# Performance work log

Measured on AMD Instinct MI355X. Metric: run time of the kernel, lower is better.

## Reference

```python
import jax, jax.numpy as jnp
import numpy as np

# Dimensions
B = 8        # batch
T = 2048     # subtokens per sample
G = 1024     # pooled tokens (nodes + edges) per sample
NN = 600     # node slots per sample (seg_ids > 0)
NE = 424     # edge slots per sample (seg_ids < 0); NN + NE == G
D = 1024     # d_model == pretrained_dim (BART-large), so need_proj is False
V = 53587    # AMRBART vocab size
L = 2        # graph_layer_configs.nlayers


def setup_inputs() -> dict:
    key = jax.random.key(0)
    ks = jax.random.split(key, 8)
    scale = 0.02
    tokens_ids = jax.random.randint(ks[0], (B, T), 0, V, dtype=jnp.int32)
    # ragged token_splits encoded as segment ids; uniform groups of size T//G == 2
    token_group_ids = jnp.broadcast_to(
        jnp.arange(T, dtype=jnp.int32) // (T // G), (B, T))
    # seg_ids: +1 for node slots, -1 for edge slots (nodes-first layout, no pad)
    seg_ids = jnp.broadcast_to(
        jnp.concatenate([jnp.ones(NN, jnp.int32), -jnp.ones(NE, jnp.int32)]),
        (B, G))
    # torch-geometric style global edge index over batch-concatenated nodes
    src = jax.random.randint(ks[1], (B, NE), 0, NN, dtype=jnp.int32)
    dst = jax.random.randint(ks[2], (B, NE), 0, NN, dtype=jnp.int32)
    offs = (jnp.arange(B, dtype=jnp.int32) * NN)[:, None]
    edge_index = jnp.stack([(src + offs).reshape(-1), (dst + offs).reshape(-1)], 0)
    embedding_table = jax.random.normal(ks[3], (V, D), dtype=jnp.float32) * scale
    W_msg = jax.random.normal(ks[4], (L, D, D), dtype=jnp.float32) * scale
    W_upd = jax.random.normal(ks[5], (L, D, D), dtype=jnp.float32) * scale
    W_edge = jax.random.normal(ks[6], (L, D, D), dtype=jnp.float32) * scale
    return {"tokens_ids": tokens_ids, "token_group_ids": token_group_ids,
            "seg_ids": seg_ids, "edge_index": edge_index,
            "embedding_table": embedding_table,
            "W_msg": W_msg, "W_upd": W_upd, "W_edge": W_edge}


def reference(tokens_ids, token_group_ids, seg_ids, edge_index,
              embedding_table, W_msg, W_upd, W_edge):
    # 1) embedding lookup: [B, T, D]
    token_feats = embedding_table[tokens_ids]
    # 2) ragged subtoken mean-pool (torch.split + mean) via segment_sum
    seg_sum = jax.vmap(lambda x, ids: jax.ops.segment_sum(x, ids, num_segments=G))
    sums = seg_sum(token_feats, token_group_ids)                       # [B, G, D]
    counts = seg_sum(jnp.ones((B, T, 1), token_feats.dtype), token_group_ids)
    pooled = sums / jnp.maximum(counts, 1.0)                           # [B, G, D]
    # 3) gather node/edge feats (seg_ids layout is nodes-first, statically known)
    nodes = pooled[:, :NN].reshape(B * NN, D)
    edges = pooled[:, NN:].reshape(B * NE, D)
    src, dst = edge_index[0], edge_index[1]
    # 4) graph layers: edge-conditioned message passing with residuals
    for l in range(L):
        msg = jax.nn.relu((nodes[src] + edges) @ W_msg[l])             # [B*NE, D]
        agg = jax.ops.segment_sum(msg, dst, num_segments=B * NN)       # [B*NN, D]
        new_edges = edges + (nodes[src] + nodes[dst]) @ W_edge[l]
        nodes = nodes + agg @ W_upd[l]
        edges = new_edges
    # 5) scatter back into padded [B, G, D] tensor (boolean-mask scatter in torch)
    all_feats = jnp.concatenate(
        [nodes.reshape(B, NN, D), edges.reshape(B, NE, D)], axis=1)
    return all_feats
```

## Files before the change

### kernel.cpp

```cpp
#include <hip/hip_runtime.h>

constexpr int kB  = 8;
constexpr int kT  = 2048;
constexpr int kG  = 1024;
constexpr int kNN = 600;
constexpr int kNE = 424;
constexpr int kD  = 1024;
constexpr int kL  = 2;
constexpr int kBNN = kB * kNN;
constexpr int kBNE = kB * kNE;
static_assert(kBNE % 64 == 0, "M tiles exact");

typedef __attribute__((ext_vector_type(4))) float f32x4;
typedef __attribute__((ext_vector_type(8))) short bf16x8;
typedef __attribute__((address_space(1))) const void gas_t;
typedef __attribute__((address_space(3))) void las_t;

__device__ __forceinline__ unsigned short f2bf(float x) {
    union { float f; unsigned u; } v; v.f = x;
    unsigned r = v.u + 0x7FFF + ((v.u >> 16) & 1);
    return (unsigned short)(r >> 16);
}

__device__ __forceinline__ void glds16(const void* g, void* l) {
    __builtin_amdgcn_global_load_lds((gas_t*)g, (las_t*)l, 16, 0, 0);
}

__device__ __forceinline__ size_t edge_out_off(int row) {
    int b = row / kNE, r = row - b * kNE;
    return ((size_t)(b * kG + kNN + r)) * kD;
}
__device__ __forceinline__ size_t node_out_off(int n) {
    int b = n / kNN, g = n - b * kNN;
    return ((size_t)(b * kG + g)) * kD;
}

__global__ __launch_bounds__(256) void prep_kernel(const int* __restrict__ tokens,
                                                   const int* __restrict__ gids,
                                                   const float* __restrict__ emb,
                                                   float* __restrict__ nodes,
                                                   float* __restrict__ edges,
                                                   const float* __restrict__ Wm,
                                                   const float* __restrict__ Wu,
                                                   const float* __restrict__ We,
                                                   unsigned short* __restrict__ Wt) {
    __shared__ float tbuf[32][33];
    int bx = blockIdx.x;
    if (bx < kB * kG) {
        int b = bx >> 10, g = bx & (kG - 1);
        int d = threadIdx.x * 4;
        const int* row = gids + (size_t)b * kT;
        int lo = 0, hi = kT;
        while (lo < hi) { int m = (lo + hi) >> 1; if (row[m] < g) lo = m + 1; else hi = m; }
        int s = lo; hi = kT;
        while (lo < hi) { int m = (lo + hi) >> 1; if (row[m] <= g) lo = m + 1; else hi = m; }
        int e = lo;
        float4 acc = make_float4(0.f, 0.f, 0.f, 0.f);
        for (int t = s; t < e; ++t) {
            int tok = tokens[(size_t)b * kT + t];
            const float4 v = *(const float4*)(emb + (size_t)tok * kD + d);
            acc.x += v.x; acc.y += v.y; acc.z += v.z; acc.w += v.w;
        }
        int c = e - s;
        float sc = 1.0f / (float)(c > 0 ? c : 1);
        acc.x *= sc; acc.y *= sc; acc.z *= sc; acc.w *= sc;
        float* dstp = (g < kNN)
            ? (nodes + (size_t)(b * kNN + g) * kD + d)
            : (edges + (size_t)(b * kNE + (g - kNN)) * kD + d);
        *(float4*)dstp = acc;
    } else {
        int idx = bx - kB * kG;
        int z = idx >> 10;
        int rem = idx & 1023;
        int n0 = (rem & 31) * 32, k0 = (rem >> 5) * 32;
        const float* W = (z < 2) ? (Wm + (size_t)z * kD * kD)
                       : (z < 4) ? (Wu + (size_t)(z - 2) * kD * kD)
                                 : (We + (size_t)(z - 4) * kD * kD);
        unsigned short* outp = Wt + (size_t)z * kD * kD;
        int r = threadIdx.x >> 3, c4 = (threadIdx.x & 7) * 4;
        const float4 v = *(const float4*)(W + (size_t)(k0 + r) * kD + n0 + c4);
        tbuf[r][c4] = v.x; tbuf[r][c4 + 1] = v.y; tbuf[r][c4 + 2] = v.z; tbuf[r][c4 + 3] = v.w;
        __syncthreads();
        ushort4 o;
        o.x = f2bf(tbuf[c4 + 0][r]); o.y = f2bf(tbuf[c4 + 1][r]);
        o.z = f2bf(tbuf[c4 + 2][r]); o.w = f2bf(tbuf[c4 + 3][r]);
        *(ushort4*)(outp + (size_t)(n0 + r) * kD + k0 + c4) = o;
    }
}

template <int COPY>
__global__ void gather_kernel(const float* __restrict__ nodes,
                              const float* __restrict__ edges,
                              const int* __restrict__ src,
                              const int* __restrict__ dst,
                              unsigned short* __restrict__ bufM,
                              unsigned short* __restrict__ bufE,
                              float* __restrict__ out) {
    int d = threadIdx.x * 4;
    int e = blockIdx.x;
    if (COPY && e >= kBNE) {
        int n = e - kBNE;
        *(float4*)(out + node_out_off(n) + d) =
            *(const float4*)(nodes + (size_t)n * kD + d);
        return;
    }
    int s = src[e], t = dst[e];
    const float4 a = *(const float4*)(nodes + (size_t)s * kD + d);
    const float4 b = *(const float4*)(edges + (size_t)e * kD + d);
    const float4 c = *(const float4*)(nodes + (size_t)t * kD + d);
    ushort4 om, oe;
    om.x = f2bf(a.x + b.x); om.y = f2bf(a.y + b.y);
    om.z = f2bf(a.z + b.z); om.w = f2bf(a.w + b.w);
    oe.x = f2bf(a.x + c.x); oe.y = f2bf(a.y + c.y);
    oe.z = f2bf(a.z + c.z); oe.w = f2bf(a.w + c.w);
    *(ushort4*)(bufM + (size_t)e * kD + d) = om;
    *(ushort4*)(bufE + (size_t)e * kD + d) = oe;
}

template <int MODE>
__device__ __forceinline__ void gemm_body(const unsigned short* __restrict__ A,
                                          const unsigned short* __restrict__ Wt,
                                          float* __restrict__ Cf,
                                          unsigned short* __restrict__ Cb,
                                          const float* __restrict__ Ef,
                                          const int* __restrict__ idxp,
                                          char* smem, int bn, int bm) {
    const int tid = threadIdx.x;
    const int lane = tid & 63;
    const int w = tid >> 6;
    const int wr = w >> 1, wc = w & 1;
    const int row0 = bm * 64, col0 = bn * 128;
    const int l15 = lane & 15, kg = lane >> 4;

    const int sl8 = lane >> 3;
    const int sc  = (lane & 7) ^ sl8;
    const unsigned short* agp[2];
    const unsigned short* bgp[4];
#pragma unroll
    for (int q = 0; q < 2; ++q)
        agp[q] = A + (size_t)(row0 + (w * 2 + q) * 8 + sl8) * kD + sc * 8;
#pragma unroll
    for (int q = 0; q < 4; ++q)
        bgp[q] = Wt + (size_t)(col0 + (w * 4 + q) * 8 + sl8) * kD + sc * 8;
    auto stage = [&](int bsel, int k0) {
        char* base = smem + bsel * 24576;
#pragma unroll
        for (int q = 0; q < 2; ++q)
            glds16(agp[q] + k0, base + (w * 2 + q) * 1024);
#pragma unroll
        for (int q = 0; q < 4; ++q)
            glds16(bgp[q] + k0, base + 8192 + (w * 4 + q) * 1024);
    };

    constexpr int nt = kD / 64;
    stage(0, 0);
    stage(1, 64);

    f32x4 acc[2][4] = {};
    for (int t = 0; t < nt; ++t) {
        char* bufc = smem + (t & 1) * 24576;
        if (t < nt - 1) asm volatile("s_waitcnt vmcnt(6)" ::: "memory");
        else            asm volatile("s_waitcnt vmcnt(0)" ::: "memory");
        __builtin_amdgcn_s_barrier();
        bf16x8 af[2][2], bf[2][4];
#pragma unroll
        for (int kk = 0; kk < 2; ++kk) {
#pragma unroll
            for (int i = 0; i < 2; ++i) {
                int ar = wr * 32 + i * 16 + l15;
                int p = ((kk << 2) | kg) ^ (ar & 7);
                af[kk][i] = *(const bf16x8*)(bufc + ar * 128 + p * 16);
            }
#pragma unroll
            for (int j = 0; j < 4; ++j) {
                int br = wc * 64 + j * 16 + l15;
                int p = ((kk << 2) | kg) ^ (br & 7);
                bf[kk][j] = *(const bf16x8*)(bufc + 8192 + br * 128 + p * 16);
            }
        }
        asm volatile("s_waitcnt lgkmcnt(0)" ::: "memory");
        __builtin_amdgcn_s_barrier();
        if (t + 2 < nt) stage(t & 1, (t + 2) * 64);
#pragma unroll
        for (int kk = 0; kk < 2; ++kk)
#pragma unroll
            for (int i = 0; i < 2; ++i)
#pragma unroll
                for (int j = 0; j < 4; ++j)
                    acc[i][j] = __builtin_amdgcn_mfma_f32_16x16x32_bf16(
                        af[kk][i], bf[kk][j], acc[i][j], 0, 0, 0);
    }
    const int lr = (lane >> 4) * 4;
#pragma unroll
    for (int i = 0; i < 2; ++i) {
        int rbase = row0 + wr * 32 + i * 16 + lr;
#pragma unroll
        for (int r = 0; r < 4; ++r) {
            int row = rbase + r;
            if (MODE == 0) {
                unsigned short* cp = Cb + (size_t)row * kD;
#pragma unroll
                for (int j = 0; j < 4; ++j) {
                    int col = col0 + wc * 64 + j * 16 + l15;
                    cp[col] = f2bf(fmaxf(acc[i][j][r], 0.f));
                }
            } else if (MODE == 1) {
                float* cp = Cf + (size_t)row * kD;
#pragma unroll
                for (int j = 0; j < 4; ++j) {
                    int col = col0 + wc * 64 + j * 16 + l15;
                    cp[col] += acc[i][j][r];
                }
            } else if (MODE == 2) {
                const float* ep = Ef + (size_t)row * kD;
                float* op = Cf + edge_out_off(row);
#pragma unroll
                for (int j = 0; j < 4; ++j) {
                    int col = col0 + wc * 64 + j * 16 + l15;
                    op[col] = ep[col] + acc[i][j][r];
                }
            } else if (MODE == 3) {
                float* cp = Cf + (size_t)idxp[row] * kD;
#pragma unroll
                for (int j = 0; j < 4; ++j) {
                    int col = col0 + wc * 64 + j * 16 + l15;
                    atomicAdd(cp + col, acc[i][j][r]);
                }
            } else {
                float* cp = Cf + node_out_off(idxp[row]);
#pragma unroll
                for (int j = 0; j < 4; ++j) {
                    int col = col0 + wc * 64 + j * 16 + l15;
                    atomicAdd(cp + col, acc[i][j][r]);
                }
            }
        }
    }
}

__global__ __launch_bounds__(256) void gemm_dual_l0(const unsigned short* __restrict__ A0,
                                                    const unsigned short* __restrict__ B0,
                                                    unsigned short* __restrict__ C0,
                                                    const unsigned short* __restrict__ A1,
                                                    const unsigned short* __restrict__ B1,
                                                    float* __restrict__ C1) {
    __shared__ char smem[49152];
    if (blockIdx.z == 0)
        gemm_body<0>(A0, B0, nullptr, C0, nullptr, nullptr, smem, blockIdx.x, blockIdx.y);
    else
        gemm_body<1>(A1, B1, C1, nullptr, nullptr, nullptr, smem, blockIdx.x, blockIdx.y);
}

__global__ __launch_bounds__(256) void gemm_dual_l1(const unsigned short* __restrict__ A0,
                                                    const unsigned short* __restrict__ B0,
                                                    unsigned short* __restrict__ C0,
                                                    const unsigned short* __restrict__ A1,
                                                    const unsigned short* __restrict__ B1,
                                                    float* __restrict__ outp,
                                                    const float* __restrict__ edges) {
    __shared__ char smem[49152];
    if (blockIdx.z == 0)
        gemm_body<0>(A0, B0, nullptr, C0, nullptr, nullptr, smem, blockIdx.x, blockIdx.y);
    else
        gemm_body<2>(A1, B1, outp, nullptr, edges, nullptr, smem, blockIdx.x, blockIdx.y);
}

__global__ __launch_bounds__(256) void gemm_upd_l0(const unsigned short* __restrict__ A,
                                                   const unsigned short* __restrict__ B,
                                                   float* __restrict__ C,
                                                   const int* __restrict__ dstIdx) {
    __shared__ char smem[49152];
    gemm_body<3>(A, B, C, nullptr, nullptr, dstIdx, smem, blockIdx.x, blockIdx.y);
}

__global__ __launch_bounds__(256) void gemm_upd_l1(const unsigned short* __restrict__ A,
                                                   const unsigned short* __restrict__ B,
                                                   float* __restrict__ outp,
                                                   const int* __restrict__ dstIdx) {
    __shared__ char smem[49152];
    gemm_body<4>(A, B, outp, nullptr, nullptr, dstIdx, smem, blockIdx.x, blockIdx.y);
}

extern "C" void kernel_launch(void* const* d_in, const int* in_sizes, int n_in,
                              void* d_out, int out_size, void* d_ws, size_t ws_size,
                              hipStream_t stream) {
    const int*   tokens = (const int*)d_in[0];
    const int*   gids   = (const int*)d_in[1];
    const int*   eidx   = (const int*)d_in[3];
    const float* emb    = (const float*)d_in[4];
    const float* Wm     = (const float*)d_in[5];
    const float* Wu     = (const float*)d_in[6];
    const float* We     = (const float*)d_in[7];
    float* out = (float*)d_out;

    constexpr size_t szNodes = (size_t)kBNN * kD * 4;
    constexpr size_t szEdges = (size_t)kBNE * kD * 4;
    constexpr size_t szBufM  = (size_t)kBNE * kD * 2;
    constexpr size_t szBufE  = (size_t)kBNE * kD * 2;
    constexpr size_t szMsgB  = (size_t)kBNE * kD * 2;
    char* ws = (char*)d_ws;
    float*          nodes = (float*)ws;
    float*          edges = (float*)(ws + szNodes);
    unsigned short* bufM  = (unsigned short*)(ws + szNodes + szEdges);
    unsigned short* bufE  = (unsigned short*)(ws + szNodes + szEdges + szBufM);
    unsigned short* msgb  = (unsigned short*)(ws + szNodes + szEdges + szBufM + szBufE);
    unsigned short* Wt    = (unsigned short*)(ws + szNodes + szEdges + szBufM + szBufE + szMsgB);

    const int* srcIdx = eidx;
    const int* dstIdx = eidx + kBNE;
    unsigned short* WtM = Wt;
    unsigned short* WtU = Wt + (size_t)2 * kD * kD;
    unsigned short* WtE = Wt + (size_t)4 * kD * kD;

    prep_kernel<<<kB * kG + 6 * 1024, 256, 0, stream>>>(
        tokens, gids, emb, nodes, edges, Wm, Wu, We, Wt);

    constexpr int mt = kBNE / 64;
    const dim3 gdual(kD / 128, mt, 2);
    const dim3 gupd(kD / 128, mt, 1);

    gather_kernel<0><<<kBNE, 256, 0, stream>>>(nodes, edges, srcIdx, dstIdx, bufM, bufE, out);
    gemm_dual_l0<<<gdual, 256, 0, stream>>>(bufM, WtM, msgb, bufE, WtE, edges);
    gemm_upd_l0<<<gupd, 256, 0, stream>>>(msgb, WtU, nodes, dstIdx);

    gather_kernel<1><<<kBNE + kBNN, 256, 0, stream>>>(nodes, edges, srcIdx, dstIdx, bufM, bufE, out);
    gemm_dual_l1<<<gdual, 256, 0, stream>>>(bufM, WtM + (size_t)kD * kD, msgb,
                                            bufE, WtE + (size_t)kD * kD, out, edges);
    gemm_upd_l1<<<gupd, 256, 0, stream>>>(msgb, WtU + (size_t)kD * kD, out, dstIdx);
}
```

Before: 148.1 us.

## Pre-swizzle weights into MFMA fragment layout and load B directly to registers

The weight transpose/convert prologue now writes bf16 weights in a per-lane MFMA fragment layout, so the GEMM loads B operands straight from global memory into registers instead of staging them through LDS. The A tile pipeline moves to a triple-buffered LDS ring with a single barrier per step and prefetched B registers. LDS use per block is halved, which can raise occupancy and cut LDS traffic. In exchange it adds register pressure and relies on the hand-tuned vmcnt counts being exact.

```diff
diff --git a/kernel.cpp b/kernel.cpp
--- a/kernel.cpp
+++ b/kernel.cpp
@@ -76,15 +76,22 @@
         const float* W = (z < 2) ? (Wm + (size_t)z * kD * kD)
                        : (z < 4) ? (Wu + (size_t)(z - 2) * kD * kD)
                                  : (We + (size_t)(z - 4) * kD * kD);
-        unsigned short* outp = Wt + (size_t)z * kD * kD;
         int r = threadIdx.x >> 3, c4 = (threadIdx.x & 7) * 4;
         const float4 v = *(const float4*)(W + (size_t)(k0 + r) * kD + n0 + c4);
         tbuf[r][c4] = v.x; tbuf[r][c4 + 1] = v.y; tbuf[r][c4 + 2] = v.z; tbuf[r][c4 + 3] = v.w;
         __syncthreads();
-        ushort4 o;
-        o.x = f2bf(tbuf[c4 + 0][r]); o.y = f2bf(tbuf[c4 + 1][r]);
-        o.z = f2bf(tbuf[c4 + 2][r]); o.w = f2bf(tbuf[c4 + 3][r]);
-        *(ushort4*)(outp + (size_t)(n0 + r) * kD + k0 + c4) = o;
+        if (threadIdx.x < 128) {
+            int f = threadIdx.x >> 6, l = threadIdx.x & 63;
+            alignas(16) unsigned short tmp[8];
+#pragma unroll
+            for (int m = 0; m < 8; ++m)
+                tmp[m] = f2bf(tbuf[(l >> 4) * 8 + m][f * 16 + (l & 15)]);
+            int nf = (rem & 31) * 2 + f;
+            int kf = rem >> 5;
+            char* dst = (char*)Wt + (size_t)z * 2097152
+                      + ((size_t)nf * 32 + kf) * 1024 + (size_t)l * 16;
+            *(float4*)dst = *(const float4*)tmp;
+        }
     }
 }
 
@@ -119,7 +126,7 @@
 
 template <int MODE>
 __device__ __forceinline__ void gemm_body(const unsigned short* __restrict__ A,
-                                          const unsigned short* __restrict__ Wt,
+                                          const unsigned short* __restrict__ Wtf,
                                           float* __restrict__ Cf,
                                           unsigned short* __restrict__ Cb,
                                           const float* __restrict__ Ef,
@@ -135,61 +142,78 @@
     const int sl8 = lane >> 3;
     const int sc  = (lane & 7) ^ sl8;
     const unsigned short* agp[2];
-    const unsigned short* bgp[4];
 #pragma unroll
     for (int q = 0; q < 2; ++q)
         agp[q] = A + (size_t)(row0 + (w * 2 + q) * 8 + sl8) * kD + sc * 8;
-#pragma unroll
-    for (int q = 0; q < 4; ++q)
-        bgp[q] = Wt + (size_t)(col0 + (w * 4 + q) * 8 + sl8) * kD + sc * 8;
     auto stage = [&](int bsel, int k0) {
-        char* base = smem + bsel * 24576;
+        char* base = smem + bsel * 8192;
 #pragma unroll
         for (int q = 0; q < 2; ++q)
             glds16(agp[q] + k0, base + (w * 2 + q) * 1024);
-#pragma unroll
-        for (int q = 0; q < 4; ++q)
-            glds16(bgp[q] + k0, base + 8192 + (w * 4 + q) * 1024);
     };
 
+    const char* bfrag[4];
+#pragma unroll
+    for (int j = 0; j < 4; ++j)
+        bfrag[j] = (const char*)Wtf
+                 + ((size_t)(bn * 8 + wc * 4 + j) * 32) * 1024 + (size_t)lane * 16;
+
     constexpr int nt = kD / 64;
+    bf16x8 bfr[2][2][4];
+
     stage(0, 0);
     stage(1, 64);
+    asm volatile("" ::: "memory");
+#pragma unroll
+    for (int kk = 0; kk < 2; ++kk)
+#pragma unroll
+        for (int j = 0; j < 4; ++j)
+            bfr[0][kk][j] = *(const bf16x8*)(bfrag[j] + (size_t)kk * 1024);
 
     f32x4 acc[2][4] = {};
-    for (int t = 0; t < nt; ++t) {
-        char* bufc = smem + (t & 1) * 24576;
-        if (t < nt - 1) asm volatile("s_waitcnt vmcnt(6)" ::: "memory");
-        else            asm volatile("s_waitcnt vmcnt(0)" ::: "memory");
-        __builtin_amdgcn_s_barrier();
-        bf16x8 af[2][2], bf[2][4];
-#pragma unroll
-        for (int kk = 0; kk < 2; ++kk) {
-#pragma unroll
-            for (int i = 0; i < 2; ++i) {
-                int ar = wr * 32 + i * 16 + l15;
-                int p = ((kk << 2) | kg) ^ (ar & 7);
-                af[kk][i] = *(const bf16x8*)(bufc + ar * 128 + p * 16);
+    for (int tt = 0; tt < nt; tt += 2) {
+#pragma unroll
+        for (int ph = 0; ph < 2; ++ph) {
+            const int t = tt + ph;
+            char* bufc = smem + (t % 3) * 8192;
+            if (t == 0)          asm volatile("s_waitcnt vmcnt(10)" ::: "memory");
+            else if (t < nt - 1) asm volatile("s_waitcnt vmcnt(18)" ::: "memory");
+            else                 asm volatile("s_waitcnt vmcnt(16)" ::: "memory");
+            __builtin_amdgcn_sched_barrier(0);
+            __builtin_amdgcn_s_barrier();
+            if (t + 2 < nt) stage((t + 2) % 3, (t + 2) * 64);
+            asm volatile("" ::: "memory");
+            if (t + 1 < nt) {
+#pragma unroll
+                for (int kk = 0; kk < 2; ++kk)
+#pragma unroll
+                    for (int j = 0; j < 4; ++j)
+                        bfr[ph ^ 1][kk][j] = *(const bf16x8*)(
+                            bfrag[j] + (size_t)((t + 1) * 2 + kk) * 1024);
             }
-#pragma unroll
-            for (int j = 0; j < 4; ++j) {
-                int br = wc * 64 + j * 16 + l15;
-                int p = ((kk << 2) | kg) ^ (br & 7);
-                bf[kk][j] = *(const bf16x8*)(bufc + 8192 + br * 128 + p * 16);
-            }
+            asm volatile("" ::: "memory");
+            bf16x8 af[2][2];
+#pragma unroll
+            for (int kk = 0; kk < 2; ++kk)
+#pragma unroll
+                for (int i = 0; i < 2; ++i) {
+                    int ar = wr * 32 + i * 16 + l15;
+                    int p = ((kk << 2) | kg) ^ (ar & 7);
+                    af[kk][i] = *(const bf16x8*)(bufc + ar * 128 + p * 16);
+                }
+            asm volatile("s_waitcnt lgkmcnt(0)" ::: "memory");
+            __builtin_amdgcn_sched_barrier(0);
+#pragma unroll
+            for (int kk = 0; kk < 2; ++kk)
+#pragma unroll
+                for (int i = 0; i < 2; ++i)
+#pragma unroll
+                    for (int j = 0; j < 4; ++j)
+                        acc[i][j] = __builtin_amdgcn_mfma_f32_16x16x32_bf16(
+                            af[kk][i], bfr[ph][kk][j], acc[i][j], 0, 0, 0);
         }
-        asm volatile("s_waitcnt lgkmcnt(0)" ::: "memory");
-        __builtin_amdgcn_s_barrier();
-        if (t + 2 < nt) stage(t & 1, (t + 2) * 64);
-#pragma unroll
-        for (int kk = 0; kk < 2; ++kk)
-#pragma unroll
-            for (int i = 0; i < 2; ++i)
-#pragma unroll
-                for (int j = 0; j < 4; ++j)
-                    acc[i][j] = __builtin_amdgcn_mfma_f32_16x16x32_bf16(
-                        af[kk][i], bf[kk][j], acc[i][j], 0, 0, 0);
     }
+
     const int lr = (lane >> 4) * 4;
 #pragma unroll
     for (int i = 0; i < 2; ++i) {
@@ -244,7 +268,7 @@
                                                     const unsigned short* __restrict__ A1,
                                                     const unsigned short* __restrict__ B1,
                                                     float* __restrict__ C1) {
-    __shared__ char smem[49152];
+    __shared__ char smem[24576];
     if (blockIdx.z == 0)
         gemm_body<0>(A0, B0, nullptr, C0, nullptr, nullptr, smem, blockIdx.x, blockIdx.y);
     else
@@ -258,7 +282,7 @@
                                                     const unsigned short* __restrict__ B1,
                                                     float* __restrict__ outp,
                                                     const float* __restrict__ edges) {
-    __shared__ char smem[49152];
+    __shared__ char smem[24576];
     if (blockIdx.z == 0)
         gemm_body<0>(A0, B0, nullptr, C0, nullptr, nullptr, smem, blockIdx.x, blockIdx.y);
     else
@@ -269,7 +293,7 @@
                                                    const unsigned short* __restrict__ B,
                                                    float* __restrict__ C,
                                                    const int* __restrict__ dstIdx) {
-    __shared__ char smem[49152];
+    __shared__ char smem[24576];
     gemm_body<3>(A, B, C, nullptr, nullptr, dstIdx, smem, blockIdx.x, blockIdx.y);
 }
 
@@ -277,7 +301,7 @@
                                                    const unsigned short* __restrict__ B,
                                                    float* __restrict__ outp,
                                                    const int* __restrict__ dstIdx) {
-    __shared__ char smem[49152];
+    __shared__ char smem[24576];
     gemm_body<4>(A, B, outp, nullptr, nullptr, dstIdx, smem, blockIdx.x, blockIdx.y);
 }
 
```

Result: slower. 166.7 us (+12.5%).
